# Performance work log

Measured on AMD Instinct MI355X. Metric: run time of the kernel, lower is better.

The kernel has to match this reference:

```python
import jax, jax.numpy as jnp
import numpy as np

B, T, I, H = 128, 2048, 2, 64


def _gru_layer(x_seq, W_ih, W_hh, b_ih, b_hh):
    """Single GRU layer, PyTorch gate convention. x_seq: [B,T,in] -> [B,T,H]."""
    # Precompute input-side gate projections for all timesteps at once.
    xg = jnp.einsum('bti,gi->btg', x_seq, W_ih) + b_ih  # [B,T,3H]

    def step(h, xg_t):
        gh = h @ W_hh.T + b_hh                     # [B,3H]
        xr, xz, xn = jnp.split(xg_t, 3, axis=-1)
        hr, hz, hn = jnp.split(gh, 3, axis=-1)
        r = jax.nn.sigmoid(xr + hr)
        z = jax.nn.sigmoid(xz + hz)
        n = jnp.tanh(xn + r * hn)
        h_new = (1.0 - z) * n + z * h
        return h_new, h_new

    h0 = jnp.zeros((x_seq.shape[0], W_hh.shape[1]), dtype=x_seq.dtype)
    _, hs = jax.lax.scan(step, h0, jnp.swapaxes(xg, 0, 1))  # scan over time
    return jnp.swapaxes(hs, 0, 1)  # [B,T,H]


def setup_inputs() -> dict:
    key = jax.random.key(0)
    ks = jax.random.split(key, 12)
    s_in = 1.0 / np.sqrt(H)
    u = lambda k, shape: jax.random.uniform(k, shape, jnp.float32, -s_in, s_in)
    return {
        'x': jax.random.normal(ks[0], (B, T, I), jnp.float32),
        'W_ih0': u(ks[1], (3 * H, I)),
        'W_hh0': u(ks[2], (3 * H, H)),
        'b_ih0': u(ks[3], (3 * H,)),
        'b_hh0': u(ks[4], (3 * H,)),
        'W_ih1': u(ks[5], (3 * H, H)),
        'W_hh1': u(ks[6], (3 * H, H)),
        'b_ih1': u(ks[7], (3 * H,)),
        'b_hh1': u(ks[8], (3 * H,)),
        'fc_w': u(ks[9], (1, H)),
        'fc_b': u(ks[10], (1,)),
    }


def reference(x, W_ih0, W_hh0, b_ih0, b_hh0, W_ih1, W_hh1, b_ih1, b_hh1, fc_w, fc_b):
    # 2-layer GRU (eval mode: inter-layer dropout inactive) + linear head.
    h1 = _gru_layer(x, W_ih0, W_hh0, b_ih0, b_hh0)    # [B,T,H]
    h2 = _gru_layer(h1, W_ih1, W_hh1, b_ih1, b_hh1)   # [B,T,H]
    out = jnp.einsum('bth,oh->bto', h2, fc_w) + fc_b  # [B,T,1]
    return out.squeeze(-1)                            # [B,T]
```

## Files before the change

kernel.cpp:

```cpp
#include <hip/hip_runtime.h>

#define BB 128
#define TT 2048
#define HH 64

typedef float2 f2;
struct f2x2 { f2 lo, hi; };

__device__ __forceinline__ float sigm(float v) {
    return __builtin_amdgcn_rcpf(1.0f + __expf(-v));
}
__device__ __forceinline__ float ftanh(float v) {
    float e = __expf(-2.0f * fabsf(v));
    float r = (1.0f - e) * __builtin_amdgcn_rcpf(1.0f + e);
    return copysignf(r, v);
}

#define PIN2(v) asm volatile("" : "+v"(v))
#define PKFMA(acc, w, h) \
    asm("v_pk_fma_f32 %0, %1, %2, %0" : "+v"(acc) : "v"(w), "v"(h))
#define SPLIT(v4, lo_, hi_) \
    { f2x2 u_ = __builtin_bit_cast(f2x2, (v4)); lo_ = u_.lo; hi_ = u_.hi; }

__device__ __forceinline__ float dppadd1(float v) {
    int s_ = __builtin_bit_cast(int, v);
    int p_ = __builtin_amdgcn_update_dpp(0, s_, 0xB1, 0xF, 0xF, true);
    return v + __builtin_bit_cast(float, p_);
}

__global__ __launch_bounds__(384)
__attribute__((amdgpu_waves_per_eu(1, 2)))
void gru_fused(const float* __restrict__ x,
               const float* __restrict__ Wih0, const float* __restrict__ Whh0,
               const float* __restrict__ bih0, const float* __restrict__ bhh0,
               const float* __restrict__ Wih1, const float* __restrict__ Whh1,
               const float* __restrict__ bih1, const float* __restrict__ bhh1,
               const float* __restrict__ fcw, const float* __restrict__ fcb,
               float* __restrict__ out)
{
    const int t  = threadIdx.x;
    const int w  = t >> 6;
    const int j  = t & 63;
    const int s  = (w < 4) ? ((w & 1) ? 2 : 0) : 1;
    const int sw = (w < 4) ? (w >> 1) : (w & 1);
    const int g  = j >> 1;
    const int q  = j & 1;
    const int d  = sw * 32 + g;
    const int b  = blockIdx.x;

    __shared__ __align__(16) float xs[TT * 2];
    __shared__ __align__(16) float h1b[2][HH];
    __shared__ __align__(16) float h2b[2][HH];
    __shared__ __align__(16) float4 xgb4[2][HH];
    __shared__ __align__(16) float fwS[HH];
    __shared__ float ring[256][65];

    const float* Wm = (s == 0) ? Whh0 : (s == 1) ? Wih1 : Whh1;
    const float4* P0 = (const float4*)(Wm + (size_t)(0 * HH + d) * HH + q * 32);
    const float4* P1 = (const float4*)(Wm + (size_t)(1 * HH + d) * HH + q * 32);
    const float4* P2 = (const float4*)(Wm + (size_t)(2 * HH + d) * HH + q * 32);
    f2 wa0, wa1, wa2, wa3, wa4, wa5, wa6, wa7,
       wa8, wa9, wa10, wa11, wa12, wa13, wa14, wa15;
    f2 wb0, wb1, wb2, wb3, wb4, wb5, wb6, wb7,
       wb8, wb9, wb10, wb11, wb12, wb13, wb14, wb15;
    f2 wc0, wc1, wc2, wc3, wc4, wc5, wc6, wc7,
       wc8, wc9, wc10, wc11, wc12, wc13, wc14, wc15;
    {
        float4 v;
        v = P0[0]; SPLIT(v, wa0,  wa1);  v = P0[1]; SPLIT(v, wa2,  wa3);
        v = P0[2]; SPLIT(v, wa4,  wa5);  v = P0[3]; SPLIT(v, wa6,  wa7);
        v = P0[4]; SPLIT(v, wa8,  wa9);  v = P0[5]; SPLIT(v, wa10, wa11);
        v = P0[6]; SPLIT(v, wa12, wa13); v = P0[7]; SPLIT(v, wa14, wa15);
        v = P1[0]; SPLIT(v, wb0,  wb1);  v = P1[1]; SPLIT(v, wb2,  wb3);
        v = P1[2]; SPLIT(v, wb4,  wb5);  v = P1[3]; SPLIT(v, wb6,  wb7);
        v = P1[4]; SPLIT(v, wb8,  wb9);  v = P1[5]; SPLIT(v, wb10, wb11);
        v = P1[6]; SPLIT(v, wb12, wb13); v = P1[7]; SPLIT(v, wb14, wb15);
        v = P2[0]; SPLIT(v, wc0,  wc1);  v = P2[1]; SPLIT(v, wc2,  wc3);
        v = P2[2]; SPLIT(v, wc4,  wc5);  v = P2[3]; SPLIT(v, wc6,  wc7);
        v = P2[4]; SPLIT(v, wc8,  wc9);  v = P2[5]; SPLIT(v, wc10, wc11);
        v = P2[6]; SPLIT(v, wc12, wc13); v = P2[7]; SPLIT(v, wc14, wc15);
    }
    PIN2(wa0);  PIN2(wa1);  PIN2(wa2);  PIN2(wa3);
    PIN2(wa4);  PIN2(wa5);  PIN2(wa6);  PIN2(wa7);
    PIN2(wa8);  PIN2(wa9);  PIN2(wa10); PIN2(wa11);
    PIN2(wa12); PIN2(wa13); PIN2(wa14); PIN2(wa15);
    PIN2(wb0);  PIN2(wb1);  PIN2(wb2);  PIN2(wb3);
    PIN2(wb4);  PIN2(wb5);  PIN2(wb6);  PIN2(wb7);
    PIN2(wb8);  PIN2(wb9);  PIN2(wb10); PIN2(wb11);
    PIN2(wb12); PIN2(wb13); PIN2(wb14); PIN2(wb15);
    PIN2(wc0);  PIN2(wc1);  PIN2(wc2);  PIN2(wc3);
    PIN2(wc4);  PIN2(wc5);  PIN2(wc6);  PIN2(wc7);
    PIN2(wc8);  PIN2(wc9);  PIN2(wc10); PIN2(wc11);
    PIN2(wc12); PIN2(wc13); PIN2(wc14); PIN2(wc15);

    float kb0, kb1, kb2, bi2 = 0.f;
    if (s == 0) {
        kb0 = bhh0[d] + bih0[d];
        kb1 = bhh0[HH + d] + bih0[HH + d];
        kb2 = bhh0[2 * HH + d];
        bi2 = bih0[2 * HH + d];
    } else if (s == 1) {
        kb0 = bih1[d]; kb1 = bih1[HH + d]; kb2 = bih1[2 * HH + d];
    } else {
        kb0 = bhh1[d]; kb1 = bhh1[HH + d]; kb2 = bhh1[2 * HH + d];
    }
    float wi0 = 0, wi1 = 0, wi2 = 0, wi3 = 0, wi4 = 0, wi5 = 0;
    if (s == 0) {
        wi0 = Wih0[d * 2];            wi1 = Wih0[d * 2 + 1];
        wi2 = Wih0[(HH + d) * 2];     wi3 = Wih0[(HH + d) * 2 + 1];
        wi4 = Wih0[(2 * HH + d) * 2]; wi5 = Wih0[(2 * HH + d) * 2 + 1];
    }
    const float fcbv = fcb[0];

    {
        const float4* xp  = (const float4*)(x + (size_t)b * TT * 2);
        float4*       xsp = (float4*)xs;
        for (int i2 = t; i2 < TT * 2 / 4; i2 += 384) xsp[i2] = xp[i2];
    }
    if (t < 2 * HH) { ((float*)h1b)[t] = 0.f; ((float*)h2b)[t] = 0.f; }
    if (t < HH) fwS[t] = fcw[t];

    float hreg = 0.f;

#define STEP(IDX, PC, PP, FL)                                                  \
    {                                                                          \
        __syncthreads();                                                       \
        const int i_ = (IDX);                                                  \
        const bool act = (s == 0) ? (i_ < TT)                                  \
                       : (s == 1) ? (i_ >= 1 && i_ <= TT)                      \
                                  : (i_ >= 2);                                 \
        if (act) {                                                             \
            const float4* hp = ((const float4*)((s < 2) ? h1b[PP] : h2b[PP])) + q * 8; \
            f2 h0, h1, h2, h3, h4, h5, h6, h7,                                 \
               h8, h9, h10, h11, h12, h13, h14, h15;                           \
            {                                                                  \
                float4 v_;                                                     \
                v_ = hp[0]; SPLIT(v_, h0,  h1);  v_ = hp[1]; SPLIT(v_, h2,  h3); \
                v_ = hp[2]; SPLIT(v_, h4,  h5);  v_ = hp[3]; SPLIT(v_, h6,  h7); \
                v_ = hp[4]; SPLIT(v_, h8,  h9);  v_ = hp[5]; SPLIT(v_, h10, h11);\
                v_ = hp[6]; SPLIT(v_, h12, h13); v_ = hp[7]; SPLIT(v_, h14, h15);\
            }                                                                  \
            f2 aR = {0.f, 0.f}, aZ = {0.f, 0.f}, aN = {0.f, 0.f};              \
            PKFMA(aR, wa0,  h0);  PKFMA(aZ, wb0,  h0);  PKFMA(aN, wc0,  h0);   \
            PKFMA(aR, wa1,  h1);  PKFMA(aZ, wb1,  h1);  PKFMA(aN, wc1,  h1);   \
            PKFMA(aR, wa2,  h2);  PKFMA(aZ, wb2,  h2);  PKFMA(aN, wc2,  h2);   \
            PKFMA(aR, wa3,  h3);  PKFMA(aZ, wb3,  h3);  PKFMA(aN, wc3,  h3);   \
            PKFMA(aR, wa4,  h4);  PKFMA(aZ, wb4,  h4);  PKFMA(aN, wc4,  h4);   \
            PKFMA(aR, wa5,  h5);  PKFMA(aZ, wb5,  h5);  PKFMA(aN, wc5,  h5);   \
            PKFMA(aR, wa6,  h6);  PKFMA(aZ, wb6,  h6);  PKFMA(aN, wc6,  h6);   \
            PKFMA(aR, wa7,  h7);  PKFMA(aZ, wb7,  h7);  PKFMA(aN, wc7,  h7);   \
            PKFMA(aR, wa8,  h8);  PKFMA(aZ, wb8,  h8);  PKFMA(aN, wc8,  h8);   \
            PKFMA(aR, wa9,  h9);  PKFMA(aZ, wb9,  h9);  PKFMA(aN, wc9,  h9);   \
            PKFMA(aR, wa10, h10); PKFMA(aZ, wb10, h10); PKFMA(aN, wc10, h10);  \
            PKFMA(aR, wa11, h11); PKFMA(aZ, wb11, h11); PKFMA(aN, wc11, h11);  \
            PKFMA(aR, wa12, h12); PKFMA(aZ, wb12, h12); PKFMA(aN, wc12, h12);  \
            PKFMA(aR, wa13, h13); PKFMA(aZ, wb13, h13); PKFMA(aN, wc13, h13);  \
            PKFMA(aR, wa14, h14); PKFMA(aZ, wb14, h14); PKFMA(aN, wc14, h14);  \
            PKFMA(aR, wa15, h15); PKFMA(aZ, wb15, h15); PKFMA(aN, wc15, h15);  \
            float sr = aR.x + aR.y, sz = aZ.x + aZ.y, sn = aN.x + aN.y;        \
            sr = dppadd1(sr); sz = dppadd1(sz); sn = dppadd1(sn);              \
            sr += kb0; sz += kb1; sn += kb2;                                   \
            if (s == 0) {                                                      \
                f2 xv = *(const f2*)(xs + 2 * i_);                             \
                float rr = sigm (fmaf(wi0, xv.x, fmaf(wi1, xv.y, sr)));        \
                float zz = sigm (fmaf(wi2, xv.x, fmaf(wi3, xv.y, sz)));        \
                float nn = ftanh(fmaf(wi4, xv.x, fmaf(wi5, xv.y, bi2)) + rr * sn); \
                hreg = (1.f - zz) * nn + zz * hreg;                            \
                if (q == 0) h1b[PC][d] = hreg;                                 \
            } else if (s == 1) {                                               \
                if (q == 0) xgb4[PP][d] = make_float4(sr, sz, sn, 0.f);        \
            } else {                                                           \
                float4 xg = xgb4[PC][d];                                       \
                float rr = sigm (xg.x + sr);                                   \
                float zz = sigm (xg.y + sz);                                   \
                float nn = ftanh(xg.z + rr * sn);                              \
                hreg = (1.f - zz) * nn + zz * hreg;                            \
                if (q == 0) {                                                  \
                    h2b[PC][d] = hreg;                                         \
                    ring[(i_ - 2) & 255][d] = hreg;                            \
                }                                                              \
            }                                                                  \
        }                                                                      \
        if (FL && w == 3 && i_ >= 66 && ((i_ - 66) & 63) == 0) {               \
            const int tt = ((i_ - 66) >> 6) * 64 + j;                          \
            const float* rr2 = ring[tt & 255];                                 \
            float acc0 = 0.f, acc1 = 0.f;                                      \
            _Pragma("unroll")                                                  \
            for (int k = 0; k < 64; k += 2) {                                  \
                acc0 += rr2[k]     * fwS[k];                                   \
                acc1 += rr2[k + 1] * fwS[k + 1];                               \
            }                                                                  \
            out[(size_t)b * TT + tt] = acc0 + acc1 + fcbv;                     \
        }                                                                      \
    }

    for (int ii = 0; ii < TT + 2; ii += 2) {
        STEP(ii,     0, 1, true);
        STEP(ii + 1, 1, 0, false);
    }
#undef STEP

    __syncthreads();
    if (w == 3) {
        const int tt = 31 * 64 + j;
        const float* rr2 = ring[tt & 255];
        float acc0 = 0.f, acc1 = 0.f;
        #pragma unroll
        for (int k = 0; k < 64; k += 2) {
            acc0 += rr2[k]     * fwS[k];
            acc1 += rr2[k + 1] * fwS[k + 1];
        }
        out[(size_t)b * TT + tt] = acc0 + acc1 + fcbv;
    }
}

extern "C" void kernel_launch(void* const* d_in, const int* in_sizes, int n_in,
                              void* d_out, int out_size, void* d_ws, size_t ws_size,
                              hipStream_t stream) {
    const float* x    = (const float*)d_in[0];
    const float* Wih0 = (const float*)d_in[1];
    const float* Whh0 = (const float*)d_in[2];
    const float* bih0 = (const float*)d_in[3];
    const float* bhh0 = (const float*)d_in[4];
    const float* Wih1 = (const float*)d_in[5];
    const float* Whh1 = (const float*)d_in[6];
    const float* bih1 = (const float*)d_in[7];
    const float* bhh1 = (const float*)d_in[8];
    const float* fcw  = (const float*)d_in[9];
    const float* fcb  = (const float*)d_in[10];
    float* out = (float*)d_out;

    gru_fused<<<BB, 384, 0, stream>>>(x, Wih0, Whh0, bih0, bhh0,
                                      Wih1, Whh1, bih1, bhh1, fcw, fcb, out);
}
```

Before: 993.8 us.

## Process two batch rows per block to reuse register-resident weights

Each block now handles two batch sequences, running the recurrent matvec and gate math for both inside each barrier-separated timestep, and the grid is halved. The intent is to amortize barrier and LDS latency over twice the work and give the scheduler independent instruction chains to interleave. The cost is a longer per-step critical path and half as many blocks, which leaves more compute units idle. The output head work moves to the two layer-1 waves, one per sequence.

```diff
diff --git a/kernel.cpp b/kernel.cpp
--- a/kernel.cpp
+++ b/kernel.cpp
@@ -46,14 +46,14 @@
     const int g  = j >> 1;
     const int q  = j & 1;
     const int d  = sw * 32 + g;
-    const int b  = blockIdx.x;
-
-    __shared__ __align__(16) float xs[TT * 2];
-    __shared__ __align__(16) float h1b[2][HH];
-    __shared__ __align__(16) float h2b[2][HH];
-    __shared__ __align__(16) float4 xgb4[2][HH];
+    const int blk = blockIdx.x;
+
+    __shared__ __align__(16) float xs[2 * TT * 2];
+    __shared__ __align__(16) float h1b[2][2][HH];
+    __shared__ __align__(16) float h2b[2][2][HH];
+    __shared__ __align__(16) float4 xgb4[2][2][HH];
     __shared__ __align__(16) float fwS[HH];
-    __shared__ float ring[256][65];
+    __shared__ float ring[2][128][65];
 
     const float* Wm = (s == 0) ? Whh0 : (s == 1) ? Wih1 : Whh1;
     const float4* P0 = (const float4*)(Wm + (size_t)(0 * HH + d) * HH + q * 32);
@@ -113,14 +113,69 @@
     const float fcbv = fcb[0];
 
     {
-        const float4* xp  = (const float4*)(x + (size_t)b * TT * 2);
+        const float4* xp  = (const float4*)(x + (size_t)(2 * blk) * TT * 2);
         float4*       xsp = (float4*)xs;
-        for (int i2 = t; i2 < TT * 2 / 4; i2 += 384) xsp[i2] = xp[i2];
-    }
-    if (t < 2 * HH) { ((float*)h1b)[t] = 0.f; ((float*)h2b)[t] = 0.f; }
+        for (int i2 = t; i2 < 2 * TT * 2 / 4; i2 += 384) xsp[i2] = xp[i2];
+    }
+    if (t < 4 * HH) { ((float*)h1b)[t] = 0.f; ((float*)h2b)[t] = 0.f; }
     if (t < HH) fwS[t] = fcw[t];
 
-    float hreg = 0.f;
+    float hreg0 = 0.f, hreg1 = 0.f;
+
+#define BATCH(bb_, hr_, i_, PC, PP)                                            \
+    {                                                                          \
+        const float4* hp = ((const float4*)((s < 2) ? h1b[PP][bb_]             \
+                                                    : h2b[PP][bb_])) + q * 8;  \
+        f2 h0, h1, h2, h3, h4, h5, h6, h7,                                     \
+           h8, h9, h10, h11, h12, h13, h14, h15;                               \
+        {                                                                      \
+            float4 v_;                                                         \
+            v_ = hp[0]; SPLIT(v_, h0,  h1);  v_ = hp[1]; SPLIT(v_, h2,  h3);   \
+            v_ = hp[2]; SPLIT(v_, h4,  h5);  v_ = hp[3]; SPLIT(v_, h6,  h7);   \
+            v_ = hp[4]; SPLIT(v_, h8,  h9);  v_ = hp[5]; SPLIT(v_, h10, h11);  \
+            v_ = hp[6]; SPLIT(v_, h12, h13); v_ = hp[7]; SPLIT(v_, h14, h15);  \
+        }                                                                      \
+        f2 aR = {0.f, 0.f}, aZ = {0.f, 0.f}, aN = {0.f, 0.f};                  \
+        PKFMA(aR, wa0,  h0);  PKFMA(aZ, wb0,  h0);  PKFMA(aN, wc0,  h0);       \
+        PKFMA(aR, wa1,  h1);  PKFMA(aZ, wb1,  h1);  PKFMA(aN, wc1,  h1);       \
+        PKFMA(aR, wa2,  h2);  PKFMA(aZ, wb2,  h2);  PKFMA(aN, wc2,  h2);       \
+        PKFMA(aR, wa3,  h3);  PKFMA(aZ, wb3,  h3);  PKFMA(aN, wc3,  h3);       \
+        PKFMA(aR, wa4,  h4);  PKFMA(aZ, wb4,  h4);  PKFMA(aN, wc4,  h4);       \
+        PKFMA(aR, wa5,  h5);  PKFMA(aZ, wb5,  h5);  PKFMA(aN, wc5,  h5);       \
+        PKFMA(aR, wa6,  h6);  PKFMA(aZ, wb6,  h6);  PKFMA(aN, wc6,  h6);       \
+        PKFMA(aR, wa7,  h7);  PKFMA(aZ, wb7,  h7);  PKFMA(aN, wc7,  h7);       \
+        PKFMA(aR, wa8,  h8);  PKFMA(aZ, wb8,  h8);  PKFMA(aN, wc8,  h8);       \
+        PKFMA(aR, wa9,  h9);  PKFMA(aZ, wb9,  h9);  PKFMA(aN, wc9,  h9);       \
+        PKFMA(aR, wa10, h10); PKFMA(aZ, wb10, h10); PKFMA(aN, wc10, h10);      \
+        PKFMA(aR, wa11, h11); PKFMA(aZ, wb11, h11); PKFMA(aN, wc11, h11);      \
+        PKFMA(aR, wa12, h12); PKFMA(aZ, wb12, h12); PKFMA(aN, wc12, h12);      \
+        PKFMA(aR, wa13, h13); PKFMA(aZ, wb13, h13); PKFMA(aN, wc13, h13);      \
+        PKFMA(aR, wa14, h14); PKFMA(aZ, wb14, h14); PKFMA(aN, wc14, h14);      \
+        PKFMA(aR, wa15, h15); PKFMA(aZ, wb15, h15); PKFMA(aN, wc15, h15);      \
+        float sr = aR.x + aR.y, sz = aZ.x + aZ.y, sn = aN.x + aN.y;            \
+        sr = dppadd1(sr); sz = dppadd1(sz); sn = dppadd1(sn);                  \
+        sr += kb0; sz += kb1; sn += kb2;                                       \
+        if (s == 0) {                                                          \
+            f2 xv = *(const f2*)(xs + bb_ * TT * 2 + 2 * i_);                  \
+            float rr = sigm (fmaf(wi0, xv.x, fmaf(wi1, xv.y, sr)));            \
+            float zz = sigm (fmaf(wi2, xv.x, fmaf(wi3, xv.y, sz)));            \
+            float nn = ftanh(fmaf(wi4, xv.x, fmaf(wi5, xv.y, bi2)) + rr * sn); \
+            hr_ = (1.f - zz) * nn + zz * hr_;                                  \
+            if (q == 0) h1b[PC][bb_][d] = hr_;                                 \
+        } else if (s == 1) {                                                   \
+            if (q == 0) xgb4[PP][bb_][d] = make_float4(sr, sz, sn, 0.f);       \
+        } else {                                                               \
+            float4 xg = xgb4[PC][bb_][d];                                      \
+            float rr = sigm (xg.x + sr);                                       \
+            float zz = sigm (xg.y + sz);                                       \
+            float nn = ftanh(xg.z + rr * sn);                                  \
+            hr_ = (1.f - zz) * nn + zz * hr_;                                  \
+            if (q == 0) {                                                      \
+                h2b[PC][bb_][d] = hr_;                                         \
+                ring[bb_][(i_ - 2) & 127][d] = hr_;                            \
+            }                                                                  \
+        }                                                                      \
+    }
 
 #define STEP(IDX, PC, PP, FL)                                                  \
     {                                                                          \
@@ -130,87 +185,43 @@
                        : (s == 1) ? (i_ >= 1 && i_ <= TT)                      \
                                   : (i_ >= 2);                                 \
         if (act) {                                                             \
-            const float4* hp = ((const float4*)((s < 2) ? h1b[PP] : h2b[PP])) + q * 8; \
-            f2 h0, h1, h2, h3, h4, h5, h6, h7,                                 \
-               h8, h9, h10, h11, h12, h13, h14, h15;                           \
-            {                                                                  \
-                float4 v_;                                                     \
-                v_ = hp[0]; SPLIT(v_, h0,  h1);  v_ = hp[1]; SPLIT(v_, h2,  h3); \
-                v_ = hp[2]; SPLIT(v_, h4,  h5);  v_ = hp[3]; SPLIT(v_, h6,  h7); \
-                v_ = hp[4]; SPLIT(v_, h8,  h9);  v_ = hp[5]; SPLIT(v_, h10, h11);\
-                v_ = hp[6]; SPLIT(v_, h12, h13); v_ = hp[7]; SPLIT(v_, h14, h15);\
-            }                                                                  \
-            f2 aR = {0.f, 0.f}, aZ = {0.f, 0.f}, aN = {0.f, 0.f};              \
-            PKFMA(aR, wa0,  h0);  PKFMA(aZ, wb0,  h0);  PKFMA(aN, wc0,  h0);   \
-            PKFMA(aR, wa1,  h1);  PKFMA(aZ, wb1,  h1);  PKFMA(aN, wc1,  h1);   \
-            PKFMA(aR, wa2,  h2);  PKFMA(aZ, wb2,  h2);  PKFMA(aN, wc2,  h2);   \
-            PKFMA(aR, wa3,  h3);  PKFMA(aZ, wb3,  h3);  PKFMA(aN, wc3,  h3);   \
-            PKFMA(aR, wa4,  h4);  PKFMA(aZ, wb4,  h4);  PKFMA(aN, wc4,  h4);   \
-            PKFMA(aR, wa5,  h5);  PKFMA(aZ, wb5,  h5);  PKFMA(aN, wc5,  h5);   \
-            PKFMA(aR, wa6,  h6);  PKFMA(aZ, wb6,  h6);  PKFMA(aN, wc6,  h6);   \
-            PKFMA(aR, wa7,  h7);  PKFMA(aZ, wb7,  h7);  PKFMA(aN, wc7,  h7);   \
-            PKFMA(aR, wa8,  h8);  PKFMA(aZ, wb8,  h8);  PKFMA(aN, wc8,  h8);   \
-            PKFMA(aR, wa9,  h9);  PKFMA(aZ, wb9,  h9);  PKFMA(aN, wc9,  h9);   \
-            PKFMA(aR, wa10, h10); PKFMA(aZ, wb10, h10); PKFMA(aN, wc10, h10);  \
-            PKFMA(aR, wa11, h11); PKFMA(aZ, wb11, h11); PKFMA(aN, wc11, h11);  \
-            PKFMA(aR, wa12, h12); PKFMA(aZ, wb12, h12); PKFMA(aN, wc12, h12);  \
-            PKFMA(aR, wa13, h13); PKFMA(aZ, wb13, h13); PKFMA(aN, wc13, h13);  \
-            PKFMA(aR, wa14, h14); PKFMA(aZ, wb14, h14); PKFMA(aN, wc14, h14);  \
-            PKFMA(aR, wa15, h15); PKFMA(aZ, wb15, h15); PKFMA(aN, wc15, h15);  \
-            float sr = aR.x + aR.y, sz = aZ.x + aZ.y, sn = aN.x + aN.y;        \
-            sr = dppadd1(sr); sz = dppadd1(sz); sn = dppadd1(sn);              \
-            sr += kb0; sz += kb1; sn += kb2;                                   \
-            if (s == 0) {                                                      \
-                f2 xv = *(const f2*)(xs + 2 * i_);                             \
-                float rr = sigm (fmaf(wi0, xv.x, fmaf(wi1, xv.y, sr)));        \
-                float zz = sigm (fmaf(wi2, xv.x, fmaf(wi3, xv.y, sz)));        \
-                float nn = ftanh(fmaf(wi4, xv.x, fmaf(wi5, xv.y, bi2)) + rr * sn); \
-                hreg = (1.f - zz) * nn + zz * hreg;                            \
-                if (q == 0) h1b[PC][d] = hreg;                                 \
-            } else if (s == 1) {                                               \
-                if (q == 0) xgb4[PP][d] = make_float4(sr, sz, sn, 0.f);        \
-            } else {                                                           \
-                float4 xg = xgb4[PC][d];                                       \
-                float rr = sigm (xg.x + sr);                                   \
-                float zz = sigm (xg.y + sz);                                   \
-                float nn = ftanh(xg.z + rr * sn);                              \
-                hreg = (1.f - zz) * nn + zz * hreg;                            \
-                if (q == 0) {                                                  \
-                    h2b[PC][d] = hreg;                                         \
-                    ring[(i_ - 2) & 255][d] = hreg;                            \
-                }                                                              \
-            }                                                                  \
-        }                                                                      \
-        if (FL && w == 3 && i_ >= 66 && ((i_ - 66) & 63) == 0) {               \
+            BATCH(0, hreg0, i_, PC, PP);                                       \
+            BATCH(1, hreg1, i_, PC, PP);                                       \
+        }                                                                      \
+        if (FL && w >= 4 && i_ >= 66 && ((i_ - 66) & 63) == 0) {               \
+            const int fb = w - 4;                                              \
             const int tt = ((i_ - 66) >> 6) * 64 + j;                          \
-            const float* rr2 = ring[tt & 255];                                 \
+            const float* rr2 = ring[fb][tt & 127];                             \
             float acc0 = 0.f, acc1 = 0.f;                                      \
             _Pragma("unroll")                                                  \
             for (int k = 0; k < 64; k += 2) {                                  \
                 acc0 += rr2[k]     * fwS[k];                                   \
                 acc1 += rr2[k + 1] * fwS[k + 1];                               \
             }                                                                  \
-            out[(size_t)b * TT + tt] = acc0 + acc1 + fcbv;                     \
-        }                                                                      \
-    }
-
+            out[(size_t)(2 * blk + fb) * TT + tt] = acc0 + acc1 + fcbv;        \
+        }                                                                      \
+    }
+
+    __syncthreads();
     for (int ii = 0; ii < TT + 2; ii += 2) {
         STEP(ii,     0, 1, true);
         STEP(ii + 1, 1, 0, false);
     }
 #undef STEP
+#undef BATCH
 
     __syncthreads();
-    if (w == 3) {
+    if (w >= 4) {
+        const int fb = w - 4;
         const int tt = 31 * 64 + j;
-        const float* rr2 = ring[tt & 255];
+        const float* rr2 = ring[fb][tt & 127];
         float acc0 = 0.f, acc1 = 0.f;
         #pragma unroll
         for (int k = 0; k < 64; k += 2) {
             acc0 += rr2[k]     * fwS[k];
             acc1 += rr2[k + 1] * fwS[k + 1];
         }
-        out[(size_t)b * TT + tt] = acc0 + acc1 + fcbv;
+        out[(size_t)(2 * blk + fb) * TT + tt] = acc0 + acc1 + fcbv;
     }
 }
 
@@ -230,6 +241,6 @@
     const float* fcb  = (const float*)d_in[10];
     float* out = (float*)d_out;
 
-    gru_fused<<<BB, 384, 0, stream>>>(x, Wih0, Whh0, bih0, bhh0,
-                                      Wih1, Whh1, bih1, bhh1, fcw, fcb, out);
-}
+    gru_fused<<<BB / 2, 384, 0, stream>>>(x, Wih0, Whh0, bih0, bhh0,
+                                          Wih1, Whh1, bih1, bhh1, fcw, fcb, out);
+}
```

New measurement: 1.638 ms. +64.8%, slower.

## Replace per-step block barriers with per-wave LDS counters and deeper buffering

Applied to the files above, without the earlier changes.

Removes the __syncthreads at every recurrence step. Each wave now publishes its completed step index to an LDS counter and spins only on the specific producer waves it depends on, with a per-dependency lag. The h1/h2/xg buffers go from 2 to 4 slots so waves can run ahead without overwriting data still being read. The loop is unrolled by 4 and the final FC flush is folded into the loop. The goal is to cut barrier latency on the serial critical path, at the cost of spin-polling overhead and trickier ordering correctness.

```diff
diff --git a/kernel.cpp b/kernel.cpp
--- a/kernel.cpp
+++ b/kernel.cpp
@@ -49,11 +49,37 @@
     const int b  = blockIdx.x;
 
     __shared__ __align__(16) float xs[TT * 2];
-    __shared__ __align__(16) float h1b[2][HH];
-    __shared__ __align__(16) float h2b[2][HH];
-    __shared__ __align__(16) float4 xgb4[2][HH];
+    __shared__ __align__(16) float h1b[4][HH];
+    __shared__ __align__(16) float h2b[4][HH];
+    __shared__ __align__(16) float4 xgb4[4][HH];
     __shared__ __align__(16) float fwS[HH];
+    __shared__ int cnt[8];
     __shared__ float ring[256][65];
+
+#define WAITUP(i_)                                                             \
+    {                                                                          \
+        const int need_ = (i_) - lagv;                                         \
+        while (true) {                                                         \
+            int c_ = (j < 6) ? __hip_atomic_load(&cnt[j], __ATOMIC_ACQUIRE,    \
+                                   __HIP_MEMORY_SCOPE_WORKGROUP)               \
+                             : 0x7fffffff;                                     \
+            if (__all(c_ >= need_)) break;                                     \
+        }                                                                      \
+    }
+#define PUBLISH(val_)                                                          \
+    if (j == 0) __hip_atomic_store(&cnt[w], (val_), __ATOMIC_RELEASE,          \
+                                   __HIP_MEMORY_SCOPE_WORKGROUP);
+
+    int lagv = 1 << 20;
+    if (s == 0) {
+        if (j == 0 || j == 2) lagv = 1;
+        else if (j == 4 || j == 5) lagv = 3;
+    } else if (s == 1) {
+        if (j == 0 || j == 2) lagv = 1;
+        else if (j == 1 || j == 3) lagv = 3;
+    } else {
+        if (j == 1 || j == 3 || j == 4 || j == 5) lagv = 1;
+    }
 
     const float* Wm = (s == 0) ? Whh0 : (s == 1) ? Wih1 : Whh1;
     const float4* P0 = (const float4*)(Wm + (size_t)(0 * HH + d) * HH + q * 32);
@@ -117,18 +143,20 @@
         float4*       xsp = (float4*)xs;
         for (int i2 = t; i2 < TT * 2 / 4; i2 += 384) xsp[i2] = xp[i2];
     }
-    if (t < 2 * HH) { ((float*)h1b)[t] = 0.f; ((float*)h2b)[t] = 0.f; }
+    if (t < 4 * HH) { ((float*)h1b)[t] = 0.f; ((float*)h2b)[t] = 0.f; }
     if (t < HH) fwS[t] = fcw[t];
+    if (t < 8) cnt[t] = -1;
+    __syncthreads();
 
     float hreg = 0.f;
 
-#define STEP(IDX, PC, PP, FL)                                                  \
+#define STEP(IDX, PC, PP, PX, FL)                                              \
     {                                                                          \
-        __syncthreads();                                                       \
         const int i_ = (IDX);                                                  \
+        WAITUP(i_);                                                            \
         const bool act = (s == 0) ? (i_ < TT)                                  \
                        : (s == 1) ? (i_ >= 1 && i_ <= TT)                      \
-                                  : (i_ >= 2);                                 \
+                                  : (i_ >= 2 && i_ <= TT + 1);                 \
         if (act) {                                                             \
             const float4* hp = ((const float4*)((s < 2) ? h1b[PP] : h2b[PP])) + q * 8; \
             f2 h0, h1, h2, h3, h4, h5, h6, h7,                                 \
@@ -170,7 +198,7 @@
             } else if (s == 1) {                                               \
                 if (q == 0) xgb4[PP][d] = make_float4(sr, sz, sn, 0.f);        \
             } else {                                                           \
-                float4 xg = xgb4[PC][d];                                       \
+                float4 xg = xgb4[PX][d];                                       \
                 float rr = sigm (xg.x + sr);                                   \
                 float zz = sigm (xg.y + sz);                                   \
                 float nn = ftanh(xg.z + rr * sn);                              \
@@ -192,26 +220,16 @@
             }                                                                  \
             out[(size_t)b * TT + tt] = acc0 + acc1 + fcbv;                     \
         }                                                                      \
-    }
-
-    for (int ii = 0; ii < TT + 2; ii += 2) {
-        STEP(ii,     0, 1, true);
-        STEP(ii + 1, 1, 0, false);
+        PUBLISH(i_);                                                           \
+    }
+
+    for (int ii = 0; ii < TT + 4; ii += 4) {
+        STEP(ii,     0, 3, 2, false);
+        STEP(ii + 1, 1, 0, 3, false);
+        STEP(ii + 2, 2, 1, 0, true);
+        STEP(ii + 3, 3, 2, 1, false);
     }
 #undef STEP
-
-    __syncthreads();
-    if (w == 3) {
-        const int tt = 31 * 64 + j;
-        const float* rr2 = ring[tt & 255];
-        float acc0 = 0.f, acc1 = 0.f;
-        #pragma unroll
-        for (int k = 0; k < 64; k += 2) {
-            acc0 += rr2[k]     * fwS[k];
-            acc1 += rr2[k + 1] * fwS[k + 1];
-        }
-        out[(size_t)b * TT + tt] = acc0 + acc1 + fcbv;
-    }
 }
 
 extern "C" void kernel_launch(void* const* d_in, const int* in_sizes, int n_in,
```

Result: slower. 1.146 ms (+15.4%).

## Merge layer-2 input and hidden projections into FP16 dot2 waves, shrink block to 256

Applied to the files above, without the earlier changes.

Layer-2 input and recurrent matvecs are merged into the same two waves, each holding both weight sets packed as FP16 pairs and using v_dot2_f32_f16. The separate xg staging through shared memory is removed. Layer-1 h and layer-2 h are mirrored into FP16 shared buffers for the dot products. The block drops from 6 waves to 4, which cuts barrier participants and per-step work imbalance. In exchange, FP16 weights and activations in layer 2 reduce accuracy, and the layer-2 waves now carry twice the arithmetic per step.

```diff
diff --git a/kernel.cpp b/kernel.cpp
--- a/kernel.cpp
+++ b/kernel.cpp
@@ -5,6 +5,8 @@
 #define HH 64
 
 typedef float2 f2;
+typedef _Float16 half_t;
+typedef half_t hf2 __attribute__((ext_vector_type(2)));
 struct f2x2 { f2 lo, hi; };
 
 __device__ __forceinline__ float sigm(float v) {
@@ -19,6 +21,10 @@
 #define PIN2(v) asm volatile("" : "+v"(v))
 #define PKFMA(acc, w, h) \
     asm("v_pk_fma_f32 %0, %1, %2, %0" : "+v"(acc) : "v"(w), "v"(h))
+#define FDOT2(acc, ws, hs) \
+    asm("v_dot2_f32_f16 %0, %1, %2, %0" : "+v"(acc) : "v"(ws), "v"(hs))
+#define PKH(dst, a, b) \
+    { hf2 t_ = {(half_t)(a), (half_t)(b)}; dst = __builtin_bit_cast(float, t_); }
 #define SPLIT(v4, lo_, hi_) \
     { f2x2 u_ = __builtin_bit_cast(f2x2, (v4)); lo_ = u_.lo; hi_ = u_.hi; }
 
@@ -28,8 +34,8 @@
     return v + __builtin_bit_cast(float, p_);
 }
 
-__global__ __launch_bounds__(384)
-__attribute__((amdgpu_waves_per_eu(1, 2)))
+__global__ __launch_bounds__(256)
+__attribute__((amdgpu_waves_per_eu(1, 1)))
 void gru_fused(const float* __restrict__ x,
                const float* __restrict__ Wih0, const float* __restrict__ Whh0,
                const float* __restrict__ bih0, const float* __restrict__ bhh0,
@@ -41,31 +47,31 @@
     const int t  = threadIdx.x;
     const int w  = t >> 6;
     const int j  = t & 63;
-    const int s  = (w < 4) ? ((w & 1) ? 2 : 0) : 1;
-    const int sw = (w < 4) ? (w >> 1) : (w & 1);
+    const int sw = w & 1;
     const int g  = j >> 1;
     const int q  = j & 1;
     const int d  = sw * 32 + g;
     const int b  = blockIdx.x;
+    const bool isA = (w < 2);
 
     __shared__ __align__(16) float xs[TT * 2];
-    __shared__ __align__(16) float h1b[2][HH];
-    __shared__ __align__(16) float h2b[2][HH];
-    __shared__ __align__(16) float4 xgb4[2][HH];
+    __shared__ __align__(16) float  h1b[2][HH];
+    __shared__ __align__(16) half_t h16[2][HH];
+    __shared__ __align__(16) half_t h2b16[2][HH];
     __shared__ __align__(16) float fwS[HH];
     __shared__ float ring[256][65];
 
-    const float* Wm = (s == 0) ? Whh0 : (s == 1) ? Wih1 : Whh1;
-    const float4* P0 = (const float4*)(Wm + (size_t)(0 * HH + d) * HH + q * 32);
-    const float4* P1 = (const float4*)(Wm + (size_t)(1 * HH + d) * HH + q * 32);
-    const float4* P2 = (const float4*)(Wm + (size_t)(2 * HH + d) * HH + q * 32);
     f2 wa0, wa1, wa2, wa3, wa4, wa5, wa6, wa7,
        wa8, wa9, wa10, wa11, wa12, wa13, wa14, wa15;
     f2 wb0, wb1, wb2, wb3, wb4, wb5, wb6, wb7,
        wb8, wb9, wb10, wb11, wb12, wb13, wb14, wb15;
     f2 wc0, wc1, wc2, wc3, wc4, wc5, wc6, wc7,
        wc8, wc9, wc10, wc11, wc12, wc13, wc14, wc15;
-    {
+
+    if (isA) {
+        const float4* P0 = (const float4*)(Whh0 + (size_t)(0 * HH + d) * HH + q * 32);
+        const float4* P1 = (const float4*)(Whh0 + (size_t)(1 * HH + d) * HH + q * 32);
+        const float4* P2 = (const float4*)(Whh0 + (size_t)(2 * HH + d) * HH + q * 32);
         float4 v;
         v = P0[0]; SPLIT(v, wa0,  wa1);  v = P0[1]; SPLIT(v, wa2,  wa3);
         v = P0[2]; SPLIT(v, wa4,  wa5);  v = P0[3]; SPLIT(v, wa6,  wa7);
@@ -79,6 +85,62 @@
         v = P2[2]; SPLIT(v, wc4,  wc5);  v = P2[3]; SPLIT(v, wc6,  wc7);
         v = P2[4]; SPLIT(v, wc8,  wc9);  v = P2[5]; SPLIT(v, wc10, wc11);
         v = P2[6]; SPLIT(v, wc12, wc13); v = P2[7]; SPLIT(v, wc14, wc15);
+    } else {
+        const float4* X0 = (const float4*)(Wih1 + (size_t)(0 * HH + d) * HH + q * 32);
+        const float4* X1 = (const float4*)(Wih1 + (size_t)(1 * HH + d) * HH + q * 32);
+        const float4* X2 = (const float4*)(Wih1 + (size_t)(2 * HH + d) * HH + q * 32);
+        const float4* H0 = (const float4*)(Whh1 + (size_t)(0 * HH + d) * HH + q * 32);
+        const float4* H1 = (const float4*)(Whh1 + (size_t)(1 * HH + d) * HH + q * 32);
+        const float4* H2 = (const float4*)(Whh1 + (size_t)(2 * HH + d) * HH + q * 32);
+        float4 v;
+        v = X0[0]; PKH(wa0.x, v.x, v.y); PKH(wa0.y, v.z, v.w);
+        v = X0[1]; PKH(wa1.x, v.x, v.y); PKH(wa1.y, v.z, v.w);
+        v = X0[2]; PKH(wa2.x, v.x, v.y); PKH(wa2.y, v.z, v.w);
+        v = X0[3]; PKH(wa3.x, v.x, v.y); PKH(wa3.y, v.z, v.w);
+        v = X0[4]; PKH(wa4.x, v.x, v.y); PKH(wa4.y, v.z, v.w);
+        v = X0[5]; PKH(wa5.x, v.x, v.y); PKH(wa5.y, v.z, v.w);
+        v = X0[6]; PKH(wa6.x, v.x, v.y); PKH(wa6.y, v.z, v.w);
+        v = X0[7]; PKH(wa7.x, v.x, v.y); PKH(wa7.y, v.z, v.w);
+        v = X1[0]; PKH(wa8.x, v.x, v.y); PKH(wa8.y, v.z, v.w);
+        v = X1[1]; PKH(wa9.x, v.x, v.y); PKH(wa9.y, v.z, v.w);
+        v = X1[2]; PKH(wa10.x, v.x, v.y); PKH(wa10.y, v.z, v.w);
+        v = X1[3]; PKH(wa11.x, v.x, v.y); PKH(wa11.y, v.z, v.w);
+        v = X1[4]; PKH(wa12.x, v.x, v.y); PKH(wa12.y, v.z, v.w);
+        v = X1[5]; PKH(wa13.x, v.x, v.y); PKH(wa13.y, v.z, v.w);
+        v = X1[6]; PKH(wa14.x, v.x, v.y); PKH(wa14.y, v.z, v.w);
+        v = X1[7]; PKH(wa15.x, v.x, v.y); PKH(wa15.y, v.z, v.w);
+        v = X2[0]; PKH(wb0.x, v.x, v.y); PKH(wb0.y, v.z, v.w);
+        v = X2[1]; PKH(wb1.x, v.x, v.y); PKH(wb1.y, v.z, v.w);
+        v = X2[2]; PKH(wb2.x, v.x, v.y); PKH(wb2.y, v.z, v.w);
+        v = X2[3]; PKH(wb3.x, v.x, v.y); PKH(wb3.y, v.z, v.w);
+        v = X2[4]; PKH(wb4.x, v.x, v.y); PKH(wb4.y, v.z, v.w);
+        v = X2[5]; PKH(wb5.x, v.x, v.y); PKH(wb5.y, v.z, v.w);
+        v = X2[6]; PKH(wb6.x, v.x, v.y); PKH(wb6.y, v.z, v.w);
+        v = X2[7]; PKH(wb7.x, v.x, v.y); PKH(wb7.y, v.z, v.w);
+        v = H0[0]; PKH(wb8.x, v.x, v.y); PKH(wb8.y, v.z, v.w);
+        v = H0[1]; PKH(wb9.x, v.x, v.y); PKH(wb9.y, v.z, v.w);
+        v = H0[2]; PKH(wb10.x, v.x, v.y); PKH(wb10.y, v.z, v.w);
+        v = H0[3]; PKH(wb11.x, v.x, v.y); PKH(wb11.y, v.z, v.w);
+        v = H0[4]; PKH(wb12.x, v.x, v.y); PKH(wb12.y, v.z, v.w);
+        v = H0[5]; PKH(wb13.x, v.x, v.y); PKH(wb13.y, v.z, v.w);
+        v = H0[6]; PKH(wb14.x, v.x, v.y); PKH(wb14.y, v.z, v.w);
+        v = H0[7]; PKH(wb15.x, v.x, v.y); PKH(wb15.y, v.z, v.w);
+        v = H1[0]; PKH(wc0.x, v.x, v.y); PKH(wc0.y, v.z, v.w);
+        v = H1[1]; PKH(wc1.x, v.x, v.y); PKH(wc1.y, v.z, v.w);
+        v = H1[2]; PKH(wc2.x, v.x, v.y); PKH(wc2.y, v.z, v.w);
+        v = H1[3]; PKH(wc3.x, v.x, v.y); PKH(wc3.y, v.z, v.w);
+        v = H1[4]; PKH(wc4.x, v.x, v.y); PKH(wc4.y, v.z, v.w);
+        v = H1[5]; PKH(wc5.x, v.x, v.y); PKH(wc5.y, v.z, v.w);
+        v = H1[6]; PKH(wc6.x, v.x, v.y); PKH(wc6.y, v.z, v.w);
+        v = H1[7]; PKH(wc7.x, v.x, v.y); PKH(wc7.y, v.z, v.w);
+        v = H2[0]; PKH(wc8.x, v.x, v.y); PKH(wc8.y, v.z, v.w);
+        v = H2[1]; PKH(wc9.x, v.x, v.y); PKH(wc9.y, v.z, v.w);
+        v = H2[2]; PKH(wc10.x, v.x, v.y); PKH(wc10.y, v.z, v.w);
+        v = H2[3]; PKH(wc11.x, v.x, v.y); PKH(wc11.y, v.z, v.w);
+        v = H2[4]; PKH(wc12.x, v.x, v.y); PKH(wc12.y, v.z, v.w);
+        v = H2[5]; PKH(wc13.x, v.x, v.y); PKH(wc13.y, v.z, v.w);
+        v = H2[6]; PKH(wc14.x, v.x, v.y); PKH(wc14.y, v.z, v.w);
+        v = H2[7]; PKH(wc15.x, v.x, v.y); PKH(wc15.y, v.z, v.w);
     }
     PIN2(wa0);  PIN2(wa1);  PIN2(wa2);  PIN2(wa3);
     PIN2(wa4);  PIN2(wa5);  PIN2(wa6);  PIN2(wa7);
@@ -93,104 +155,137 @@
     PIN2(wc8);  PIN2(wc9);  PIN2(wc10); PIN2(wc11);
     PIN2(wc12); PIN2(wc13); PIN2(wc14); PIN2(wc15);
 
-    float kb0, kb1, kb2, bi2 = 0.f;
-    if (s == 0) {
+    float kb0 = 0, kb1 = 0, kb2 = 0, bi2 = 0;
+    float kbx0 = 0, kbx1 = 0, kbx2 = 0;
+    float kbh0 = 0, kbh1 = 0, kbh2 = 0;
+    float wi0 = 0, wi1 = 0, wi2 = 0, wi3 = 0, wi4 = 0, wi5 = 0;
+    if (isA) {
         kb0 = bhh0[d] + bih0[d];
         kb1 = bhh0[HH + d] + bih0[HH + d];
         kb2 = bhh0[2 * HH + d];
         bi2 = bih0[2 * HH + d];
-    } else if (s == 1) {
-        kb0 = bih1[d]; kb1 = bih1[HH + d]; kb2 = bih1[2 * HH + d];
-    } else {
-        kb0 = bhh1[d]; kb1 = bhh1[HH + d]; kb2 = bhh1[2 * HH + d];
-    }
-    float wi0 = 0, wi1 = 0, wi2 = 0, wi3 = 0, wi4 = 0, wi5 = 0;
-    if (s == 0) {
         wi0 = Wih0[d * 2];            wi1 = Wih0[d * 2 + 1];
         wi2 = Wih0[(HH + d) * 2];     wi3 = Wih0[(HH + d) * 2 + 1];
         wi4 = Wih0[(2 * HH + d) * 2]; wi5 = Wih0[(2 * HH + d) * 2 + 1];
+    } else {
+        kbx0 = bih1[d]; kbx1 = bih1[HH + d]; kbx2 = bih1[2 * HH + d];
+        kbh0 = bhh1[d]; kbh1 = bhh1[HH + d]; kbh2 = bhh1[2 * HH + d];
     }
     const float fcbv = fcb[0];
 
     {
         const float4* xp  = (const float4*)(x + (size_t)b * TT * 2);
         float4*       xsp = (float4*)xs;
-        for (int i2 = t; i2 < TT * 2 / 4; i2 += 384) xsp[i2] = xp[i2];
-    }
-    if (t < 2 * HH) { ((float*)h1b)[t] = 0.f; ((float*)h2b)[t] = 0.f; }
+        for (int i2 = t; i2 < TT * 2 / 4; i2 += 256) xsp[i2] = xp[i2];
+    }
+    if (t < 2 * HH) {
+        ((float*)h1b)[t] = 0.f;
+        ((half_t*)h16)[t]   = (half_t)0.f;
+        ((half_t*)h2b16)[t] = (half_t)0.f;
+    }
     if (t < HH) fwS[t] = fcw[t];
 
     float hreg = 0.f;
+    float xro = 0.f, xzo = 0.f, xno = 0.f;
+
+#define ROW16(acc, S0,S1,S2,S3,S4,S5,S6,S7, ZA,ZB,ZC,ZD)                       \
+    FDOT2(acc, S0.x, ZA.x); FDOT2(acc, S0.y, ZA.y);                            \
+    FDOT2(acc, S1.x, ZA.z); FDOT2(acc, S1.y, ZA.w);                            \
+    FDOT2(acc, S2.x, ZB.x); FDOT2(acc, S2.y, ZB.y);                            \
+    FDOT2(acc, S3.x, ZB.z); FDOT2(acc, S3.y, ZB.w);                            \
+    FDOT2(acc, S4.x, ZC.x); FDOT2(acc, S4.y, ZC.y);                            \
+    FDOT2(acc, S5.x, ZC.z); FDOT2(acc, S5.y, ZC.w);                            \
+    FDOT2(acc, S6.x, ZD.x); FDOT2(acc, S6.y, ZD.y);                            \
+    FDOT2(acc, S7.x, ZD.z); FDOT2(acc, S7.y, ZD.w);
 
 #define STEP(IDX, PC, PP, FL)                                                  \
     {                                                                          \
         __syncthreads();                                                       \
         const int i_ = (IDX);                                                  \
-        const bool act = (s == 0) ? (i_ < TT)                                  \
-                       : (s == 1) ? (i_ >= 1 && i_ <= TT)                      \
-                                  : (i_ >= 2);                                 \
-        if (act) {                                                             \
-            const float4* hp = ((const float4*)((s < 2) ? h1b[PP] : h2b[PP])) + q * 8; \
-            f2 h0, h1, h2, h3, h4, h5, h6, h7,                                 \
-               h8, h9, h10, h11, h12, h13, h14, h15;                           \
-            {                                                                  \
-                float4 v_;                                                     \
-                v_ = hp[0]; SPLIT(v_, h0,  h1);  v_ = hp[1]; SPLIT(v_, h2,  h3); \
-                v_ = hp[2]; SPLIT(v_, h4,  h5);  v_ = hp[3]; SPLIT(v_, h6,  h7); \
-                v_ = hp[4]; SPLIT(v_, h8,  h9);  v_ = hp[5]; SPLIT(v_, h10, h11);\
-                v_ = hp[6]; SPLIT(v_, h12, h13); v_ = hp[7]; SPLIT(v_, h14, h15);\
-            }                                                                  \
-            f2 aR = {0.f, 0.f}, aZ = {0.f, 0.f}, aN = {0.f, 0.f};              \
-            PKFMA(aR, wa0,  h0);  PKFMA(aZ, wb0,  h0);  PKFMA(aN, wc0,  h0);   \
-            PKFMA(aR, wa1,  h1);  PKFMA(aZ, wb1,  h1);  PKFMA(aN, wc1,  h1);   \
-            PKFMA(aR, wa2,  h2);  PKFMA(aZ, wb2,  h2);  PKFMA(aN, wc2,  h2);   \
-            PKFMA(aR, wa3,  h3);  PKFMA(aZ, wb3,  h3);  PKFMA(aN, wc3,  h3);   \
-            PKFMA(aR, wa4,  h4);  PKFMA(aZ, wb4,  h4);  PKFMA(aN, wc4,  h4);   \
-            PKFMA(aR, wa5,  h5);  PKFMA(aZ, wb5,  h5);  PKFMA(aN, wc5,  h5);   \
-            PKFMA(aR, wa6,  h6);  PKFMA(aZ, wb6,  h6);  PKFMA(aN, wc6,  h6);   \
-            PKFMA(aR, wa7,  h7);  PKFMA(aZ, wb7,  h7);  PKFMA(aN, wc7,  h7);   \
-            PKFMA(aR, wa8,  h8);  PKFMA(aZ, wb8,  h8);  PKFMA(aN, wc8,  h8);   \
-            PKFMA(aR, wa9,  h9);  PKFMA(aZ, wb9,  h9);  PKFMA(aN, wc9,  h9);   \
-            PKFMA(aR, wa10, h10); PKFMA(aZ, wb10, h10); PKFMA(aN, wc10, h10);  \
-            PKFMA(aR, wa11, h11); PKFMA(aZ, wb11, h11); PKFMA(aN, wc11, h11);  \
-            PKFMA(aR, wa12, h12); PKFMA(aZ, wb12, h12); PKFMA(aN, wc12, h12);  \
-            PKFMA(aR, wa13, h13); PKFMA(aZ, wb13, h13); PKFMA(aN, wc13, h13);  \
-            PKFMA(aR, wa14, h14); PKFMA(aZ, wb14, h14); PKFMA(aN, wc14, h14);  \
-            PKFMA(aR, wa15, h15); PKFMA(aZ, wb15, h15); PKFMA(aN, wc15, h15);  \
-            float sr = aR.x + aR.y, sz = aZ.x + aZ.y, sn = aN.x + aN.y;        \
-            sr = dppadd1(sr); sz = dppadd1(sz); sn = dppadd1(sn);              \
-            sr += kb0; sz += kb1; sn += kb2;                                   \
-            if (s == 0) {                                                      \
+        if (isA) {                                                             \
+            if (i_ < TT) {                                                     \
+                const float4* hp = ((const float4*)h1b[PP]) + q * 8;           \
+                f2 h0, h1, h2, h3, h4, h5, h6, h7,                             \
+                   h8, h9, h10, h11, h12, h13, h14, h15;                       \
+                {                                                              \
+                    float4 v_;                                                 \
+                    v_ = hp[0]; SPLIT(v_, h0,  h1);  v_ = hp[1]; SPLIT(v_, h2,  h3); \
+                    v_ = hp[2]; SPLIT(v_, h4,  h5);  v_ = hp[3]; SPLIT(v_, h6,  h7); \
+                    v_ = hp[4]; SPLIT(v_, h8,  h9);  v_ = hp[5]; SPLIT(v_, h10, h11);\
+                    v_ = hp[6]; SPLIT(v_, h12, h13); v_ = hp[7]; SPLIT(v_, h14, h15);\
+                }                                                              \
+                f2 aR = {0.f, 0.f}, aZ = {0.f, 0.f}, aN = {0.f, 0.f};          \
+                PKFMA(aR, wa0,  h0);  PKFMA(aZ, wb0,  h0);  PKFMA(aN, wc0,  h0);   \
+                PKFMA(aR, wa1,  h1);  PKFMA(aZ, wb1,  h1);  PKFMA(aN, wc1,  h1);   \
+                PKFMA(aR, wa2,  h2);  PKFMA(aZ, wb2,  h2);  PKFMA(aN, wc2,  h2);   \
+                PKFMA(aR, wa3,  h3);  PKFMA(aZ, wb3,  h3);  PKFMA(aN, wc3,  h3);   \
+                PKFMA(aR, wa4,  h4);  PKFMA(aZ, wb4,  h4);  PKFMA(aN, wc4,  h4);   \
+                PKFMA(aR, wa5,  h5);  PKFMA(aZ, wb5,  h5);  PKFMA(aN, wc5,  h5);   \
+                PKFMA(aR, wa6,  h6);  PKFMA(aZ, wb6,  h6);  PKFMA(aN, wc6,  h6);   \
+                PKFMA(aR, wa7,  h7);  PKFMA(aZ, wb7,  h7);  PKFMA(aN, wc7,  h7);   \
+                PKFMA(aR, wa8,  h8);  PKFMA(aZ, wb8,  h8);  PKFMA(aN, wc8,  h8);   \
+                PKFMA(aR, wa9,  h9);  PKFMA(aZ, wb9,  h9);  PKFMA(aN, wc9,  h9);   \
+                PKFMA(aR, wa10, h10); PKFMA(aZ, wb10, h10); PKFMA(aN, wc10, h10);  \
+                PKFMA(aR, wa11, h11); PKFMA(aZ, wb11, h11); PKFMA(aN, wc11, h11);  \
+                PKFMA(aR, wa12, h12); PKFMA(aZ, wb12, h12); PKFMA(aN, wc12, h12);  \
+                PKFMA(aR, wa13, h13); PKFMA(aZ, wb13, h13); PKFMA(aN, wc13, h13);  \
+                PKFMA(aR, wa14, h14); PKFMA(aZ, wb14, h14); PKFMA(aN, wc14, h14);  \
+                PKFMA(aR, wa15, h15); PKFMA(aZ, wb15, h15); PKFMA(aN, wc15, h15);  \
+                float sr = aR.x + aR.y, sz = aZ.x + aZ.y, sn = aN.x + aN.y;    \
+                sr = dppadd1(sr); sz = dppadd1(sz); sn = dppadd1(sn);          \
+                sr += kb0; sz += kb1; sn += kb2;                               \
                 f2 xv = *(const f2*)(xs + 2 * i_);                             \
                 float rr = sigm (fmaf(wi0, xv.x, fmaf(wi1, xv.y, sr)));        \
                 float zz = sigm (fmaf(wi2, xv.x, fmaf(wi3, xv.y, sz)));        \
                 float nn = ftanh(fmaf(wi4, xv.x, fmaf(wi5, xv.y, bi2)) + rr * sn); \
                 hreg = (1.f - zz) * nn + zz * hreg;                            \
-                if (q == 0) h1b[PC][d] = hreg;                                 \
-            } else if (s == 1) {                                               \
-                if (q == 0) xgb4[PP][d] = make_float4(sr, sz, sn, 0.f);        \
-            } else {                                                           \
-                float4 xg = xgb4[PC][d];                                       \
-                float rr = sigm (xg.x + sr);                                   \
-                float zz = sigm (xg.y + sz);                                   \
-                float nn = ftanh(xg.z + rr * sn);                              \
+                if (q == 0) {                                                  \
+                    h1b[PC][d] = hreg;                                         \
+                    h16[PC][d] = (half_t)hreg;                                 \
+                }                                                              \
+            }                                                                  \
+        } else {                                                               \
+            float axr = 0.f, axz = 0.f, axn = 0.f;                             \
+            const bool doX = (i_ >= 1 && i_ <= TT);                            \
+            if (doX) {                          \
+                const float4* zp = ((const float4*)h16[PP]) + q * 4;           \
+                float4 Z0 = zp[0], Z1 = zp[1], Z2 = zp[2], Z3 = zp[3];         \
+                ROW16(axr, wa0, wa1, wa2,  wa3,  wa4,  wa5,  wa6,  wa7,  Z0, Z1, Z2, Z3); \
+                ROW16(axz, wa8, wa9, wa10, wa11, wa12, wa13, wa14, wa15, Z0, Z1, Z2, Z3); \
+                ROW16(axn, wb0, wb1, wb2,  wb3,  wb4,  wb5,  wb6,  wb7,  Z0, Z1, Z2, Z3); \
+                axr = dppadd1(axr); axz = dppadd1(axz); axn = dppadd1(axn);    \
+            }                                                                  \
+            if (i_ >= 2) {                  \
+                const float4* yp = ((const float4*)h2b16[PP]) + q * 4;         \
+                float4 Y0 = yp[0], Y1 = yp[1], Y2 = yp[2], Y3 = yp[3];         \
+                float ahr = 0.f, ahz = 0.f, ahn = 0.f;                         \
+                ROW16(ahr, wb8, wb9, wb10, wb11, wb12, wb13, wb14, wb15, Y0, Y1, Y2, Y3); \
+                ROW16(ahz, wc0, wc1, wc2,  wc3,  wc4,  wc5,  wc6,  wc7,  Y0, Y1, Y2, Y3); \
+                ROW16(ahn, wc8, wc9, wc10, wc11, wc12, wc13, wc14, wc15, Y0, Y1, Y2, Y3); \
+                ahr = dppadd1(ahr) + kbh0;                                     \
+                ahz = dppadd1(ahz) + kbh1;                                     \
+                ahn = dppadd1(ahn) + kbh2;                                     \
+                float rr = sigm (xro + ahr);                                   \
+                float zz = sigm (xzo + ahz);                                   \
+                float nn = ftanh(xno + rr * ahn);                              \
                 hreg = (1.f - zz) * nn + zz * hreg;                            \
                 if (q == 0) {                                                  \
-                    h2b[PC][d] = hreg;                                         \
+                    h2b16[PC][d] = (half_t)hreg;                               \
                     ring[(i_ - 2) & 255][d] = hreg;                            \
                 }                                                              \
             }                                                                  \
-        }                                                                      \
-        if (FL && w == 3 && i_ >= 66 && ((i_ - 66) & 63) == 0) {               \
-            const int tt = ((i_ - 66) >> 6) * 64 + j;                          \
-            const float* rr2 = ring[tt & 255];                                 \
-            float acc0 = 0.f, acc1 = 0.f;                                      \
-            _Pragma("unroll")                                                  \
-            for (int k = 0; k < 64; k += 2) {                                  \
-                acc0 += rr2[k]     * fwS[k];                                   \
-                acc1 += rr2[k + 1] * fwS[k + 1];                               \
+            if (doX) { xro = axr + kbx0; xzo = axz + kbx1; xno = axn + kbx2; } \
+            if (FL && w == 3 && i_ >= 66 && ((i_ - 66) & 63) == 0) {           \
+                const int tt = ((i_ - 66) >> 6) * 64 + j;                      \
+                const float* rr2 = ring[tt & 255];                             \
+                float acc0 = 0.f, acc1 = 0.f;                                  \
+                _Pragma("unroll")                                              \
+                for (int k = 0; k < 64; k += 2) {                              \
+                    acc0 += rr2[k]     * fwS[k];                               \
+                    acc1 += rr2[k + 1] * fwS[k + 1];                           \
+                }                                                              \
+                out[(size_t)b * TT + tt] = acc0 + acc1 + fcbv;                 \
             }                                                                  \
-            out[(size_t)b * TT + tt] = acc0 + acc1 + fcbv;                     \
         }                                                                      \
     }
 
@@ -199,6 +294,7 @@
         STEP(ii + 1, 1, 0, false);
     }
 #undef STEP
+#undef ROW16
 
     __syncthreads();
     if (w == 3) {
@@ -230,6 +326,6 @@
     const float* fcb  = (const float*)d_in[10];
     float* out = (float*)d_out;
 
-    gru_fused<<<BB, 384, 0, stream>>>(x, Wih0, Whh0, bih0, bhh0,
+    gru_fused<<<BB, 256, 0, stream>>>(x, Wih0, Whh0, bih0, bhh0,
                                       Wih1, Whh1, bih1, bhh1, fcw, fcb, out);
 }
```

After: 1.011 ms. About the same (+1.7%).
